# Optimization experiments

Measured on AMD Instinct MI355X. Metric: run time of the kernel, lower is better.

The kernel has to match this reference:

```python
import jax, jax.numpy as jnp
import numpy as np

N = 50000; E = 800000; G = 256; F = 34; D = 128; H = 4; C = 32; L = 4
EPS = 1e-5

def _bn(x, g, b):
    # BatchNorm1d with batch statistics (train-mode math), eval dropout (identity)
    m = jnp.mean(x, 0); v = jnp.var(x, 0)
    return g * (x - m) * jax.lax.rsqrt(v + EPS) + b

def _seg_softmax(s, seg, n):
    # numerically-stable softmax over edges grouped by destination node
    m = jax.ops.segment_max(s, seg, num_segments=n)
    m = jnp.where(jnp.isfinite(m), m, 0.0)
    e = jnp.exp(s - m[seg])
    d = jax.ops.segment_sum(e, seg, num_segments=n)
    return e / (d[seg] + 1e-16)

def setup_inputs():
    key = jax.random.key(0)
    ks = iter(jax.random.split(key, 64))
    def rn(shape, s=0.05):
        return jax.random.normal(next(ks), shape, dtype=jnp.float32) * s
    inp = {}
    inp['x'] = jax.random.normal(next(ks), (N, F), dtype=jnp.float32)
    inp['edge_index'] = jax.random.randint(next(ks), (2, E), 0, N, dtype=jnp.int32)
    inp['batch'] = jnp.sort(jax.random.randint(next(ks), (N,), 0, G, dtype=jnp.int32))
    inp['emb_W'] = rn((F, D)); inp['emb_b'] = rn((D,))
    inp['emb_g'] = jnp.ones((D,)); inp['emb_be'] = jnp.zeros((D,))
    inp['gWl'] = rn((L, D, D)); inp['gWr'] = rn((L, D, D))
    inp['gbl'] = rn((L, D)); inp['gbr'] = rn((L, D))
    inp['gatt'] = rn((L, H, C)); inp['gbias'] = rn((L, D))
    inp['gg'] = jnp.ones((L, D)); inp['gbe'] = jnp.zeros((L, D))
    inp['tWq'] = rn((D, D)); inp['tWk'] = rn((D, D)); inp['tWv'] = rn((D, D)); inp['tWs'] = rn((D, D))
    inp['tbq'] = rn((D,)); inp['tbk'] = rn((D,)); inp['tbv'] = rn((D,)); inp['tbs'] = rn((D,))
    inp['tg'] = jnp.ones((D,)); inp['tbe'] = jnp.zeros((D,))
    inp['oW1'] = rn((2 * D, D)); inp['ob1'] = rn((D,))
    inp['og'] = jnp.ones((D,)); inp['obe'] = jnp.zeros((D,))
    inp['oW2'] = rn((D, D // 2)); inp['ob2'] = rn((D // 2,))
    inp['oW3'] = rn((D // 2, 1)); inp['ob3'] = rn((1,))
    return inp

def reference(x, edge_index, batch, emb_W, emb_b, emb_g, emb_be, gWl, gWr, gbl, gbr, gatt, gbias, gg, gbe, tWq, tWk, tWv, tWs, tbq, tbk, tbv, tbs, tg, tbe, oW1, ob1, og, obe, oW2, ob2, oW3, ob3):
    x = jax.nn.relu(_bn(x @ emb_W + emb_b, emb_g, emb_be))
    sl = jnp.arange(N, dtype=edge_index.dtype)
    ei = jnp.concatenate([edge_index, jnp.stack([sl, sl])], axis=1)  # GATv2 default add_self_loops=True
    src, dst = ei[0], ei[1]
    for l in range(L):  # 4 structurally identical GATv2 layers
        xl = (x @ gWl[l] + gbl[l]).reshape(N, H, C)
        xr = (x @ gWr[l] + gbr[l]).reshape(N, H, C)
        e = jax.nn.leaky_relu(xl[src] + xr[dst], 0.2)  # [E+N, H, C]
        sc = jnp.einsum('ehc,hc->eh', e, gatt[l])
        a = _seg_softmax(sc, dst, N)
        out = jax.ops.segment_sum(xl[src] * a[..., None], dst, num_segments=N).reshape(N, D) + gbias[l]
        x = x + jax.nn.relu(_bn(out, gg[l], gbe[l]))
    # TransformerConv: no self-loops by default, dot-product attention + root skip
    s2, d2 = edge_index[0], edge_index[1]
    q = (x @ tWq + tbq).reshape(N, H, C)
    k = (x @ tWk + tbk).reshape(N, H, C)
    v = (x @ tWv + tbv).reshape(N, H, C)
    sc = jnp.einsum('ehc,ehc->eh', q[d2], k[s2]) / np.float32(np.sqrt(C))
    a = _seg_softmax(sc, d2, N)
    agg = jax.ops.segment_sum(v[s2] * a[..., None], d2, num_segments=N).reshape(N, D)
    x = x + _bn(agg + x @ tWs + tbs, tg, tbe)
    # global mean + max pooling over graphs
    cnt = jax.ops.segment_sum(jnp.ones((N,), x.dtype), batch, num_segments=G)
    xm = jax.ops.segment_sum(x, batch, num_segments=G) / jnp.maximum(cnt, 1.0)[:, None]
    xx = jax.ops.segment_max(x, batch, num_segments=G)
    xx = jnp.where(jnp.isfinite(xx), xx, 0.0)  # guard empty segments
    h = jnp.concatenate([xm, xx], axis=1)
    h = jax.nn.relu(_bn(h @ oW1 + ob1, og, obe))
    h = jax.nn.relu(h @ oW2 + ob2)
    return h @ oW3 + ob3
```

## Files before the change

kernel.cpp:

```cpp
#include <hip/hip_runtime.h>
#include <hip/hip_fp16.h>

namespace {
constexpr int NN = 50000;
constexpr int NE = 800000;
constexpr int NG = 256;
constexpr int NF = 34;
constexpr int NL = 4;
constexpr int NB = (NN + 255) / 256;
}
#define EPSB 1e-5f
#define LSLOPE 0.2f
#define INV_SQRT_C 0.17677669529663687f

typedef short bf16x8 __attribute__((ext_vector_type(8)));
typedef float f32x4 __attribute__((ext_vector_type(4)));
typedef _Float16 hv2 __attribute__((ext_vector_type(2)));

static __device__ __forceinline__ short f2bf(float f) {
    unsigned int u = __float_as_uint(f);
    u = (u + 0x7fff + ((u >> 16) & 1)) >> 16;
    return (short)u;
}
static __device__ __forceinline__ unsigned fenc(float x) {
    unsigned u = __float_as_uint(x);
    return (u & 0x80000000u) ? ~u : (u | 0x80000000u);
}
static __device__ __forceinline__ float fdec(unsigned u) {
    return __uint_as_float((u & 0x80000000u) ? (u ^ 0x80000000u) : ~u);
}
static __device__ __forceinline__ float fdot2(hv2 a, hv2 b, float c) {
    return __builtin_amdgcn_fdot2(a, b, c, false);
}

__global__ __launch_bounds__(256) void k_deg(const int* __restrict__ ei,
                                             int* __restrict__ deg,
                                             int* __restrict__ rank) {
    int tid = blockIdx.x * 256 + threadIdx.x;
    const int S = (NE + 3) / 4;
    if (tid >= S) return;
#pragma unroll
    for (int k = 0; k < 4; ++k) {
// ... 22 lines not shown
    sm[t] = v;
    __syncthreads();
    for (int off = 1; off < 256; off <<= 1) {
        int u = (t >= off) ? sm[t - off] : 0;
        __syncthreads();
        sm[t] += u;
        __syncthreads();
    }
    if (t < NB) boff[t] = sm[t] - v;
    if (t == 255) rp[NN] = sm[255];
}

__global__ __launch_bounds__(256) void k_scan3(const int* __restrict__ deg,
                                               const int* __restrict__ boff,
                                               int* __restrict__ rp) {
    __shared__ int sm[256];
    int i = blockIdx.x * 256 + threadIdx.x;
    int t = threadIdx.x;
    int v = (i < NN) ? deg[i] : 0;
    sm[t] = v;
    __syncthreads();
    for (int off = 1; off < 256; off <<= 1) {
        int u = (t >= off) ? sm[t - off] : 0;
        __syncthreads();
        sm[t] += u;
        __syncthreads();
    }
    if (i < NN) rp[i] = boff[blockIdx.x] + sm[t] - v;
}

__global__ __launch_bounds__(256) void k_fill(const int* __restrict__ ei,
                                              const int* __restrict__ rp,
                                              const int* __restrict__ rank,
                                              int2* __restrict__ edg) {
    int tid = blockIdx.x * 256 + threadIdx.x;
    const int S = (NE + 3) / 4;
    if (tid >= S) return;
#pragma unroll
    for (int k = 0; k < 4; ++k) {
        int e = tid + k * S;
        if (e < NE) {
            int s = ei[e];
            int d = ei[NE + e];
            int p = rp[d] + rank[e];
            edg[p] = make_int2(s, d);
        }
    }
}

__global__ __launch_bounds__(256) void k_prep(const float* __restrict__ gWl,
                                              const float* __restrict__ gWr,
                                              const float* __restrict__ tWq,
                                              const float* __restrict__ tWk,
                                              const float* __restrict__ tWv,
                                              const float* __restrict__ tWs,
                                              short* __restrict__ dst) {
    int m = blockIdx.x;
    const float* src;
    if (m < 4) src = gWl + m * 16384;
    else if (m < 8) src = gWr + (m - 4) * 16384;
    else if (m == 8) src = tWq;
    else if (m == 9) src = tWk;
    else if (m == 10) src = tWv;
    else src = tWs;
    short* d = dst + m * 16384;
    for (int i = threadIdx.x; i < 16384; i += 256) {
        int n = i >> 7, k = i & 127;
        d[i] = f2bf(src[k * 128 + n]);
    }
}

template <int OUTH0, int OUTH1, int RES, int XOUT>
__global__ __launch_bounds__(256) void k_gemm2bn(const float* __restrict__ src,
                                                 const float* __restrict__ res,
                                                 float* __restrict__ xout,
                                                 const float* __restrict__ st,
                                                 const float* __restrict__ g,
                                                 const float* __restrict__ b,
                                                 const short* __restrict__ Wt0,
                                                 const short* __restrict__ Wt1,
                                                 const float* __restrict__ bias0,
                                                 const float* __restrict__ bias1,
                                                 void* __restrict__ out0,
                                                 void* __restrict__ out1, int nRows) {
    __shared__ short As[128 * 136];
    __shared__ short Bs[128 * 136];
    __shared__ float scsh[256];
    const float invn = 1.f / NN;
    if (threadIdx.x < 128) {
        int c = threadIdx.x;
        float mean = st[c] * invn;
        float var = fmaxf(st[128 + c] * invn - mean * mean, 0.f);
        float s = g[c] * rsqrtf(var + EPSB);
        scsh[c] = s;
        scsh[128 + c] = b[c] - mean * s;
    }
    {
        const int4* Wt4 = (const int4*)Wt0;
        for (int idx = threadIdx.x; idx < 2048; idx += 256) {
            int row = idx >> 4, c8 = idx & 15;
            *(int4*)&Bs[row * 136 + c8 * 8] = Wt4[idx];
        }
    }
    __syncthreads();
    int r0 = blockIdx.x * 128;
    int rows = nRows - r0; if (rows > 128) rows = 128;
    for (int idx = threadIdx.x; idx < 2048; idx += 256) {
        int r = idx >> 4, c8 = idx & 15;
        short4 sa = {0, 0, 0, 0}, sb = {0, 0, 0, 0};
        if (r < rows) {
            size_t base = (size_t)(r0 + r) * 128 + c8 * 8;
            float4 v0 = *(const float4*)&src[base];
            float4 v1 = *(const float4*)&src[base + 4];
            int c = c8 * 8;
            v0.x = fmaxf(v0.x * scsh[c + 0] + scsh[128 + c + 0], 0.f);
            v0.y = fmaxf(v0.y * scsh[c + 1] + scsh[128 + c + 1], 0.f);
            v0.z = fmaxf(v0.z * scsh[c + 2] + scsh[128 + c + 2], 0.f);
            v0.w = fmaxf(v0.w * scsh[c + 3] + scsh[128 + c + 3], 0.f);
            v1.x = fmaxf(v1.x * scsh[c + 4] + scsh[128 + c + 4], 0.f);
            v1.y = fmaxf(v1.y * scsh[c + 5] + scsh[128 + c + 5], 0.f);
            v1.z = fmaxf(v1.z * scsh[c + 6] + scsh[128 + c + 6], 0.f);
            v1.w = fmaxf(v1.w * scsh[c + 7] + scsh[128 + c + 7], 0.f);
            if (RES) {
                float4 rr0 = *(const float4*)&res[base];
                float4 rr1 = *(const float4*)&res[base + 4];
// ... 79 lines not shown
#pragma unroll
            for (int reg = 0; reg < 4; ++reg) {
                int r = wave * 32 + rt * 16 + quad * 4 + reg;
                if (r < rows) {
                    float v = acc[rt][ct][reg] + bv;
                    if (OUTH1) ((__half*)out1)[(size_t)(r0 + r) * 128 + colI] = __float2half(v);
                    else       ((float*)out1)[(size_t)(r0 + r) * 128 + colI] = v;
                }
            }
    }
}

__global__ __launch_bounds__(256) void k_gemm4bn(const float* __restrict__ src,
                                                 const float* __restrict__ res,
                                                 float* __restrict__ xout,
                                                 const float* __restrict__ st,
                                                 const float* __restrict__ g,
                                                 const float* __restrict__ b,
                                                 const short* __restrict__ Wt,
                                                 const float* __restrict__ bq,
                                                 const float* __restrict__ bk,
                                                 const float* __restrict__ bv,
                                                 const float* __restrict__ bs,
                                                 __half* __restrict__ oq,
                                                 __half* __restrict__ ok,
                                                 __half* __restrict__ ov,
                                                 __half* __restrict__ os, int nRows) {
    __shared__ short As[128 * 136];
    __shared__ short Bs[128 * 136];
    __shared__ float scsh[256];
    const float invn = 1.f / NN;
    if (threadIdx.x < 128) {
        int c = threadIdx.x;
        float mean = st[c] * invn;
        float var = fmaxf(st[128 + c] * invn - mean * mean, 0.f);
        float s = g[c] * rsqrtf(var + EPSB);
        scsh[c] = s;
        scsh[128 + c] = b[c] - mean * s;
    }
    __syncthreads();
    int r0 = blockIdx.x * 128;
    int rows = nRows - r0; if (rows > 128) rows = 128;
    for (int idx = threadIdx.x; idx < 2048; idx += 256) {
        int r = idx >> 4, c8 = idx & 15;
        short4 sa = {0, 0, 0, 0}, sb = {0, 0, 0, 0};
        if (r < rows) {
            size_t base = (size_t)(r0 + r) * 128 + c8 * 8;
            float4 v0 = *(const float4*)&src[base];
            float4 v1 = *(const float4*)&src[base + 4];
            int c = c8 * 8;
            v0.x = fmaxf(v0.x * scsh[c + 0] + scsh[128 + c + 0], 0.f);
            v0.y = fmaxf(v0.y * scsh[c + 1] + scsh[128 + c + 1], 0.f);
            v0.z = fmaxf(v0.z * scsh[c + 2] + scsh[128 + c + 2], 0.f);
            v0.w = fmaxf(v0.w * scsh[c + 3] + scsh[128 + c + 3], 0.f);
            v1.x = fmaxf(v1.x * scsh[c + 4] + scsh[128 + c + 4], 0.f);
            v1.y = fmaxf(v1.y * scsh[c + 5] + scsh[128 + c + 5], 0.f);
            v1.z = fmaxf(v1.z * scsh[c + 6] + scsh[128 + c + 6], 0.f);
            v1.w = fmaxf(v1.w * scsh[c + 7] + scsh[128 + c + 7], 0.f);
            float4 rr0 = *(const float4*)&res[base];
            float4 rr1 = *(const float4*)&res[base + 4];
            v0.x += rr0.x; v0.y += rr0.y; v0.z += rr0.z; v0.w += rr0.w;
            v1.x += rr1.x; v1.y += rr1.y; v1.z += rr1.z; v1.w += rr1.w;
            *(float4*)&xout[base] = v0;
            *(float4*)&xout[base + 4] = v1;
            sa.x = f2bf(v0.x); sa.y = f2bf(v0.y); sa.z = f2bf(v0.z); sa.w = f2bf(v0.w);
            sb.x = f2bf(v1.x); sb.y = f2bf(v1.y); sb.z = f2bf(v1.z); sb.w = f2bf(v1.w);
        }
        *(short4*)&As[r * 136 + c8 * 8] = sa;
// ... 27 lines not shown
        for (int rt = 0; rt < 2; ++rt)
#pragma unroll
            for (int ct = 0; ct < 8; ++ct) acc[rt][ct] = (f32x4){0.f, 0.f, 0.f, 0.f};
#pragma unroll
        for (int ct = 0; ct < 8; ++ct)
#pragma unroll
            for (int kc = 0; kc < 4; ++kc) {
                bf16x8 bf = *(const bf16x8*)&Bs[(ct * 16 + n16) * 136 + kc * 32 + quad * 8];
                acc[0][ct] = __builtin_amdgcn_mfma_f32_16x16x32_bf16(af[0][kc], bf, acc[0][ct], 0, 0, 0);
                acc[1][ct] = __builtin_amdgcn_mfma_f32_16x16x32_bf16(af[1][kc], bf, acc[1][ct], 0, 0, 0);
            }
        __half* om = outs[m];
        const float* bm = biases[m];
#pragma unroll
        for (int ct = 0; ct < 8; ++ct) {
            int colI = ct * 16 + n16;
            float bv2 = bm[colI];
#pragma unroll
            for (int rt = 0; rt < 2; ++rt)
#pragma unroll
                for (int reg = 0; reg < 4; ++reg) {
                    int r = wave * 32 + rt * 16 + quad * 4 + reg;
                    if (r < rows)
                        om[(size_t)(r0 + r) * 128 + colI] = __float2half(acc[rt][ct][reg] + bv2);
                }
        }
        if (m < 3) __syncthreads();
    }
}

__global__ __launch_bounds__(256) void k_gemm_emb(const float* __restrict__ A,
                                                  const float* __restrict__ W,
                                                  const float* __restrict__ bias,
                                                  float* __restrict__ out, int nRows) {
    __shared__ float As[64 * NF];
    int r0 = blockIdx.x * 64;
    int rows = nRows - r0; if (rows > 64) rows = 64;
    int total = rows * NF;
    for (int idx = threadIdx.x; idx < 64 * NF; idx += 256)
        As[idx] = (idx < total) ? A[(size_t)r0 * NF + idx] : 0.f;
    __syncthreads();
    int tx = threadIdx.x & 31, ty = threadIdx.x >> 5;
    const float4* W4 = (const float4*)W;
    float acc[8][4];
#pragma unroll
    for (int j = 0; j < 8; ++j)
#pragma unroll
        for (int i = 0; i < 4; ++i) acc[j][i] = 0.f;
#pragma unroll 2
    for (int k = 0; k < NF; ++k) {
        float4 w = W4[k * 32 + tx];
#pragma unroll
        for (int j = 0; j < 8; ++j) {
            float a = As[(ty * 8 + j) * NF + k];
            acc[j][0] += a * w.x; acc[j][1] += a * w.y;
            acc[j][2] += a * w.z; acc[j][3] += a * w.w;
        }
    }
    float4 b = ((const float4*)bias)[tx];
#pragma unroll
    for (int j = 0; j < 8; ++j) {
        int r = ty * 8 + j;
        if (r < rows) {
            float4 o = make_float4(acc[j][0] + b.x, acc[j][1] + b.y,
                                   acc[j][2] + b.z, acc[j][3] + b.w);
            ((float4*)out)[(size_t)(r0 + r) * 32 + tx] = o;
        }
    }
}

__global__ __launch_bounds__(256) void k_stats(const float* __restrict__ src, int nRows,
                                               float* __restrict__ st) {
    int c = threadIdx.x & 127;
    int sub = threadIdx.x >> 7;
    int r0 = blockIdx.x * 128;
    int rend = r0 + 128; if (rend > nRows) rend = nRows;
    float s = 0.f, ss = 0.f;
    for (int r = r0 + sub; r < rend; r += 2) {
        float v = src[(size_t)r * 128 + c];
        s += v; ss += v * v;
    }
    atomicAdd(&st[c], s);
    atomicAdd(&st[128 + c], ss);
}

__global__ __launch_bounds__(256) void k_gat_aggr(const __half* __restrict__ xl,
                                                  const __half* __restrict__ xr,
                                                  const float* __restrict__ att,
                                                  const float* __restrict__ gbias_l,
                                                  const int* __restrict__ rp,
                                                  const int2* __restrict__ edg,
                                                  float* __restrict__ out) {
    int lane = threadIdx.x & 63;
    int node = blockIdx.x * 4 + (threadIdx.x >> 6);
    if (node >= NN) return;
    int q = lane >> 4;
    int l16 = lane & 15;
    int c8 = l16 * 8;
    float4 xrr = *(const float4*)&xr[(unsigned)node * 128u + c8];
    hv2 xrh[4] = {*(hv2*)&xrr.x, *(hv2*)&xrr.y, *(hv2*)&xrr.z, *(hv2*)&xrr.w};
    float4 atA = *(const float4*)&att[c8];
    float4 atB = *(const float4*)&att[c8 + 4];
    hv2 ath[4] = {{(_Float16)atA.x, (_Float16)atA.y}, {(_Float16)atA.z, (_Float16)atA.w},
                  {(_Float16)atB.x, (_Float16)atB.y}, {(_Float16)atB.z, (_Float16)atB.w}};
    const hv2 hz = {(_Float16)0.f, (_Float16)0.f};
    const hv2 hs = {(_Float16)LSLOPE, (_Float16)LSLOPE};
    int s0 = rp[node];
    int T = rp[node + 1] - s0 + 1;
    float a[8] = {0.f, 0.f, 0.f, 0.f, 0.f, 0.f, 0.f, 0.f};
    float l = 0.f;
    auto body = [&](int j) {
        bool self = (j == T - 1);
        int src = self ? node : edg[s0 + j].x;
        float4 raw = *(const float4*)&xl[(unsigned)src * 128u + c8];
        hv2 f[4] = {*(hv2*)&raw.x, *(hv2*)&raw.y, *(hv2*)&raw.z, *(hv2*)&raw.w};
        float p = 0.f;
#pragma unroll
        for (int k = 0; k < 4; ++k) {
            hv2 e = f[k] + xrh[k];
            hv2 lk = __builtin_elementwise_max(e, hz) + hs * __builtin_elementwise_min(e, hz);
            p = fdot2(lk, ath[k], p);
        }
        p += __shfl_xor(p, 1); p += __shfl_xor(p, 2);
        float w = __expf(p);
#pragma unroll
        for (int k = 0; k < 4; ++k) {
            a[2 * k] += w * (float)f[k].x;
            a[2 * k + 1] += w * (float)f[k].y;
        }
        l += w;
    };
    int j = q;
    for (; j + 4 < T; j += 8) { body(j); body(j + 4); }
    for (; j < T; j += 4) body(j);
#pragma unroll
    for (int k = 0; k < 8; ++k) { a[k] += __shfl_xor(a[k], 16); a[k] += __shfl_xor(a[k], 32); }
    l += __shfl_xor(l, 16); l += __shfl_xor(l, 32);
    if (q == 0) {
        float inv = 1.f / (l + 1e-16f);
        float4 gb0 = *(const float4*)&gbias_l[c8];
        float4 gb1 = *(const float4*)&gbias_l[c8 + 4];
        float4 o0 = make_float4(a[0] * inv + gb0.x, a[1] * inv + gb0.y,
                                a[2] * inv + gb0.z, a[3] * inv + gb0.w);
        float4 o1 = make_float4(a[4] * inv + gb1.x, a[5] * inv + gb1.y,
                                a[6] * inv + gb1.z, a[7] * inv + gb1.w);
        *(float4*)&out[(unsigned)node * 128u + c8] = o0;
        *(float4*)&out[(unsigned)node * 128u + c8 + 4] = o1;
    }
}

__global__ __launch_bounds__(256) void k_trans_aggr(const __half* __restrict__ qh,
                                                    const __half* __restrict__ kh,
                                                    const __half* __restrict__ vv,
                                                    const __half* __restrict__ sT,
                                                    const int* __restrict__ rp,
                                                    const int2* __restrict__ edg,
                                                    float* __restrict__ out) {
    int lane = threadIdx.x & 63;
    int node = blockIdx.x * 4 + (threadIdx.x >> 6);
    if (node >= NN) return;
    int q = lane >> 4;
    int l16 = lane & 15;
    int c8 = l16 * 8;
    float4 qr = *(const float4*)&qh[(unsigned)node * 128u + c8];
    const hv2 hinv = {(_Float16)INV_SQRT_C, (_Float16)INV_SQRT_C};
    hv2 qv[4] = {(*(hv2*)&qr.x) * hinv, (*(hv2*)&qr.y) * hinv,
                 (*(hv2*)&qr.z) * hinv, (*(hv2*)&qr.w) * hinv};
    int s0 = rp[node];
    int T = rp[node + 1] - s0;
    float a[8] = {0.f, 0.f, 0.f, 0.f, 0.f, 0.f, 0.f, 0.f};
    float l = 0.f;
    auto body = [&](int j) {
        int src = edg[s0 + j].x;
        float4 kraw = *(const float4*)&kh[(unsigned)src * 128u + c8];
        float4 vraw = *(const float4*)&vv[(unsigned)src * 128u + c8];
        hv2 kv[4] = {*(hv2*)&kraw.x, *(hv2*)&kraw.y, *(hv2*)&kraw.z, *(hv2*)&kraw.w};
        float p = 0.f;
#pragma unroll
        for (int k = 0; k < 4; ++k) p = fdot2(kv[k], qv[k], p);
        p += __shfl_xor(p, 1); p += __shfl_xor(p, 2);
        float w = __expf(p);
        hv2 vvv[4] = {*(hv2*)&vraw.x, *(hv2*)&vraw.y, *(hv2*)&vraw.z, *(hv2*)&vraw.w};
#pragma unroll
        for (int k = 0; k < 4; ++k) {
            a[2 * k] += w * (float)vvv[k].x;
            a[2 * k + 1] += w * (float)vvv[k].y;
        }
        l += w;
    };
    int j = q;
    for (; j + 4 < T; j += 8) { body(j); body(j + 4); }
    for (; j < T; j += 4) body(j);
#pragma unroll
    for (int k = 0; k < 8; ++k) { a[k] += __shfl_xor(a[k], 16); a[k] += __shfl_xor(a[k], 32); }
    l += __shfl_xor(l, 16); l += __shfl_xor(l, 32);
    if (q == 0) {
        float inv = 1.f / (l + 1e-16f);
        float4 straw = *(const float4*)&sT[(unsigned)node * 128u + c8];
        hv2 st[4] = {*(hv2*)&straw.x, *(hv2*)&straw.y, *(hv2*)&straw.z, *(hv2*)&straw.w};
        float4 o0 = make_float4(a[0] * inv + (float)st[0].x, a[1] * inv + (float)st[0].y,
                                a[2] * inv + (float)st[1].x, a[3] * inv + (float)st[1].y);
        float4 o1 = make_float4(a[4] * inv + (float)st[2].x, a[5] * inv + (float)st[2].y,
                                a[6] * inv + (float)st[3].x, a[7] * inv + (float)st[3].y);
        *(float4*)&out[(unsigned)node * 128u + c8] = o0;
        *(float4*)&out[(unsigned)node * 128u + c8 + 4] = o1;
    }
}

__global__ __launch_bounds__(256) void k_pool_part(const float* __restrict__ src,
                                                   const float* __restrict__ res,
                                                   const float* __restrict__ st,
                                                   const float* __restrict__ g,
                                                   const float* __restrict__ b,
                                                   const int* __restrict__ batch,
                                                   float* __restrict__ psum,
                                                   unsigned* __restrict__ pmax) {
    __shared__ int bs[64];
    int r0 = blockIdx.x * 64;
    if (threadIdx.x < 64) {
        int r = r0 + threadIdx.x;
        bs[threadIdx.x] = (r < NN) ? batch[r] : -1;
    }
    __syncthreads();
    int c = threadIdx.x & 127;
    int sub = threadIdx.x >> 7;
    const float invn = 1.f / NN;
    float mean = st[c] * invn;
    float var = fmaxf(st[128 + c] * invn - mean * mean, 0.f);
    float scv = g[c] * rsqrtf(var + EPSB);
    float shv = b[c] - mean * scv;
    int curg = -1;
    float s = 0.f, fmx = -INFINITY;
    for (int i = sub; i < 64; i += 2) {
        int r = r0 + i;
        if (r >= NN) break;
        int gr = bs[i];
        if (gr != curg) {
            if (curg >= 0) {
                atomicAdd(&psum[curg * 128 + c], s);
                atomicMax(&pmax[curg * 128 + c], fenc(fmx));
            }
            curg = gr; s = 0.f; fmx = -INFINITY;
        }
        float v = src[(size_t)r * 128 + c] * scv + shv + res[(size_t)r * 128 + c];
        s += v; fmx = fmaxf(fmx, v);
    }
    if (curg >= 0) {
        atomicAdd(&psum[curg * 128 + c], s);
        atomicMax(&pmax[curg * 128 + c], fenc(fmx));
    }
}

__global__ __launch_bounds__(128) void k_pool_final(const float* __restrict__ psum,
                                                    const unsigned* __restrict__ pmax,
                                                    const int* __restrict__ batch,
                                                    float* __restrict__ h) {
    __shared__ int se[2];
    int g = blockIdx.x;
    if (threadIdx.x == 0) {
        int lo = 0, hi = NN;
        while (lo < hi) { int mid = (lo + hi) >> 1; if (batch[mid] < g) lo = mid + 1; else hi = mid; }
        se[0] = lo;
        hi = NN;
        while (lo < hi) { int mid = (lo + hi) >> 1; if (batch[mid] < g + 1) lo = mid + 1; else hi = mid; }
        se[1] = lo;
    }
    __syncthreads();
    int cnt = se[1] - se[0];
    int c = threadIdx.x;
    float xm = psum[g * 128 + c] / fmaxf((float)cnt, 1.f);
    float xx = (cnt > 0) ? fdec(pmax[g * 128 + c]) : 0.f;
    h[g * 256 + c] = xm;
    h[g * 256 + 128 + c] = xx;
}

__global__ __launch_bounds__(128) void k_head1(const float* __restrict__ h,
                                               const float* __restrict__ W,
                                               const float* __restrict__ b,
                                               float* __restrict__ t1) {
    __shared__ float hr[256];
    int row = blockIdx.x;
    int t = threadIdx.x;
    hr[t] = h[row * 256 + t];
    hr[t + 128] = h[row * 256 + 128 + t];
    __syncthreads();
    float acc = b[t];
#pragma unroll 4
    for (int k = 0; k < 256; ++k) acc += hr[k] * W[k * 128 + t];
    t1[row * 128 + t] = acc;
}

__global__ __launch_bounds__(64) void k_head2(const float* __restrict__ t1,
                                              const float* __restrict__ st,
                                              const float* __restrict__ og,
                                              const float* __restrict__ obe,
                                              const float* __restrict__ W2,
                                              const float* __restrict__ b2,
                                              const float* __restrict__ W3,
                                              const float* __restrict__ b3,
                                              float* __restrict__ out) {
    __shared__ float v[128];
    int row = blockIdx.x, t = threadIdx.x;
    const float invn = 1.f / NG;
#pragma unroll
    for (int half = 0; half < 2; ++half) {
        int ch = t + half * 64;
        float mean = st[ch] * invn;
        float var = fmaxf(st[128 + ch] * invn - mean * mean, 0.f);
        float scv = og[ch] * rsqrtf(var + EPSB);
        float shv = obe[ch] - mean * scv;
        float a = t1[row * 128 + ch] * scv + shv;
        v[ch] = fmaxf(a, 0.f);
    }
    __syncthreads();
    float acc = b2[t];
#pragma unroll 4
    for (int k = 0; k < 128; ++k) acc += v[k] * W2[k * 64 + t];
    float p = fmaxf(acc, 0.f) * W3[t];
    p += __shfl_xor(p, 1); p += __shfl_xor(p, 2); p += __shfl_xor(p, 4);
    p += __shfl_xor(p, 8); p += __shfl_xor(p, 16); p += __shfl_xor(p, 32);
    if (t == 0) out[row] = p + b3[0];
}
// ... 28 lines not shown
    const float* tbe    = (const float*)d_in[24];
    const float* oW1    = (const float*)d_in[25];
    const float* ob1    = (const float*)d_in[26];
    const float* og     = (const float*)d_in[27];
    const float* obe    = (const float*)d_in[28];
    const float* oW2    = (const float*)d_in[29];
    const float* ob2    = (const float*)d_in[30];
    const float* oW3    = (const float*)d_in[31];
    const float* ob3    = (const float*)d_in[32];
    float* out = (float*)d_out;

    const size_t NDsz = (size_t)NN * 128;
    float* x     = (float*)d_ws;
    float* bA    = x + NDsz;
    float* bC    = bA + NDsz;
    float* stats = bC + NDsz;
    float* hpool = stats + 7 * 256;
    float* t1    = hpool + 65536;
    float* scb   = t1 + 32768;
    __half* xlh  = (__half*)(scb + (size_t)(NE + NN) * 4);
    __half* xrh  = xlh + NDsz;
    __half* vh   = xrh + NDsz;
    __half* sh   = vh + NDsz;
    short* Wt    = (short*)(sh + NDsz);
    int* deg     = (int*)(Wt + 12 * 16384);
    int* rp      = deg + NN;
    int* cursor  = rp + NN + 1;
    int2* edg    = (int2*)(cursor + NN);
    int* bsum    = (int*)(edg + NE + 64);
    int* boff    = bsum + 256;
    float* psum  = (float*)(boff + 256);
    unsigned* pmax = (unsigned*)(psum + NG * 128);
    int* rank    = (int*)scb;

    hipMemsetAsync(deg, 0, NN * sizeof(int), stream);
    hipMemsetAsync(stats, 0, 7 * 256 * sizeof(float), stream);
    hipMemsetAsync(psum, 0, NG * 128 * 2 * sizeof(float), stream);

    k_prep<<<12, 256, 0, stream>>>(gWl, gWr, tWq, tWk, tWv, tWs, Wt);

    const int S4 = (NE + 3) / 4;
    const int gQuarter = (S4 + 255) / 256;
    k_deg<<<gQuarter, 256, 0, stream>>>(ei, deg, rank);
    k_scan1<<<NB, 256, 0, stream>>>(deg, bsum);
    k_scan2<<<1, 256, 0, stream>>>(bsum, boff, rp);
    k_scan3<<<NB, 256, 0, stream>>>(deg, boff, rp);
    k_fill<<<gQuarter, 256, 0, stream>>>(ei, rp, rank, edg);

    const int gEmb  = (NN + 63) / 64;
    const int gGemm = (NN + 127) / 128;
    const int gStat = (NN + 127) / 128;
    const int gNode = (NN + 3) / 4;
    const int gPool = (NN + 63) / 64;

    k_gemm_emb<<<gEmb, 256, 0, stream>>>(x_in, emb_W, emb_b, bA, NN);
    k_stats<<<gStat, 256, 0, stream>>>(bA, NN, stats);

    k_gemm2bn<1, 1, 0, 1><<<gGemm, 256, 0, stream>>>(bA, nullptr, x, stats, emb_g, emb_be,
                                                     Wt + (size_t)0 * 16384, Wt + (size_t)4 * 16384,
                                                     gbl + 0 * 128, gbr + 0 * 128, xlh, xrh, NN);
    k_gat_aggr<<<gNode, 256, 0, stream>>>(xlh, xrh, gatt + 0 * 128, gbias + 0 * 128, rp, edg, bC);
    k_stats<<<gStat, 256, 0, stream>>>(bC, NN, stats + 1 * 256);
    k_gemm2bn<1, 1, 1, 1><<<gGemm, 256, 0, stream>>>(bC, x, bA, stats + 1 * 256, gg + 0 * 128, gbe + 0 * 128,
                                                     Wt + (size_t)1 * 16384, Wt + (size_t)5 * 16384,
                                                     gbl + 1 * 128, gbr + 1 * 128, xlh, xrh, NN);
    k_gat_aggr<<<gNode, 256, 0, stream>>>(xlh, xrh, gatt + 1 * 128, gbias + 1 * 128, rp, edg, bC);
    k_stats<<<gStat, 256, 0, stream>>>(bC, NN, stats + 2 * 256);
    k_gemm2bn<1, 1, 1, 1><<<gGemm, 256, 0, stream>>>(bC, bA, x, stats + 2 * 256, gg + 1 * 128, gbe + 1 * 128,
                                                     Wt + (size_t)2 * 16384, Wt + (size_t)6 * 16384,
                                                     gbl + 2 * 128, gbr + 2 * 128, xlh, xrh, NN);
    k_gat_aggr<<<gNode, 256, 0, stream>>>(xlh, xrh, gatt + 2 * 128, gbias + 2 * 128, rp, edg, bC);
    k_stats<<<gStat, 256, 0, stream>>>(bC, NN, stats + 3 * 256);
    k_gemm2bn<1, 1, 1, 1><<<gGemm, 256, 0, stream>>>(bC, x, bA, stats + 3 * 256, gg + 2 * 128, gbe + 2 * 128,
                                                     Wt + (size_t)3 * 16384, Wt + (size_t)7 * 16384,
                                                     gbl + 3 * 128, gbr + 3 * 128, xlh, xrh, NN);
    k_gat_aggr<<<gNode, 256, 0, stream>>>(xlh, xrh, gatt + 3 * 128, gbias + 3 * 128, rp, edg, bC);
    k_stats<<<gStat, 256, 0, stream>>>(bC, NN, stats + 4 * 256);

    k_gemm4bn<<<gGemm, 256, 0, stream>>>(bC, bA, x, stats + 4 * 256, gg + 3 * 128, gbe + 3 * 128,
                                         Wt + (size_t)8 * 16384, tbq, tbk, tbv, tbs,
                                         xrh, xlh, vh, sh, NN);
    k_trans_aggr<<<gNode, 256, 0, stream>>>(xrh, xlh, vh, sh, rp, edg, bC);
    k_stats<<<gStat, 256, 0, stream>>>(bC, NN, stats + 5 * 256);

    k_pool_part<<<gPool, 256, 0, stream>>>(bC, x, stats + 5 * 256, tg, tbe, batch, psum, pmax);
    k_pool_final<<<NG, 128, 0, stream>>>(psum, pmax, batch, hpool);
    k_head1<<<NG, 128, 0, stream>>>(hpool, oW1, ob1, t1);
    k_stats<<<(NG + 127) / 128, 256, 0, stream>>>(t1, NG, stats + 6 * 256);
    k_head2<<<NG, 64, 0, stream>>>(t1, stats + 6 * 256, og, obe, oW2, ob2, oW3, ob3, out);
}
```

Before: 921.9 us.

## Fuse BatchNorm statistics into producer kernels and compact edge list

Removes the separate k_stats passes by accumulating per-channel sum and sum-of-squares inside the embedding GEMM, GAT aggregation, transformer aggregation and head1 kernels. Partial sums are spread over 32 strided slots to reduce atomic contention, and consumers reduce those slots. The CSR edge array stores only source indices, which the aggregation kernels load 64 at a time and broadcast by shuffle. Pool-final and head1 are merged. This saves re-reading the 50000x128 activations several times and some launches, at the cost of extra shared-memory atomics and a block-wide sync in the aggregation kernels.

```diff
diff --git a/kernel.cpp b/kernel.cpp
--- a/kernel.cpp
+++ b/kernel.cpp
@@ -8,6 +8,7 @@
 constexpr int NF = 34;
 constexpr int NL = 4;
 constexpr int NB = (NN + 255) / 256;
+constexpr int STS = 32;
 }
 #define EPSB 1e-5f
 #define LSLOPE 0.2f
@@ -96,7 +97,7 @@
 __global__ __launch_bounds__(256) void k_fill(const int* __restrict__ ei,
                                               const int* __restrict__ rp,
                                               const int* __restrict__ rank,
-                                              int2* __restrict__ edg) {
+                                              int* __restrict__ esrc) {
     int tid = blockIdx.x * 256 + threadIdx.x;
     const int S = (NE + 3) / 4;
     if (tid >= S) return;
@@ -107,7 +108,7 @@
             int s = ei[e];
             int d = ei[NE + e];
             int p = rp[d] + rank[e];
-            edg[p] = make_int2(s, d);
+            esrc[p] = s;
         }
     }
 }
@@ -153,8 +154,14 @@
     const float invn = 1.f / NN;
     if (threadIdx.x < 128) {
         int c = threadIdx.x;
-        float mean = st[c] * invn;
-        float var = fmaxf(st[128 + c] * invn - mean * mean, 0.f);
+        float s0v = 0.f, s1v = 0.f;
+#pragma unroll 8
+        for (int k2 = 0; k2 < STS; ++k2) {
+            s0v += st[k2 * 256 + c];
+            s1v += st[k2 * 256 + 128 + c];
+        }
+        float mean = s0v * invn;
+        float var = fmaxf(s1v * invn - mean * mean, 0.f);
         float s = g[c] * rsqrtf(var + EPSB);
         scsh[c] = s;
         scsh[128 + c] = b[c] - mean * s;
@@ -300,8 +307,14 @@
     const float invn = 1.f / NN;
     if (threadIdx.x < 128) {
         int c = threadIdx.x;
-        float mean = st[c] * invn;
-        float var = fmaxf(st[128 + c] * invn - mean * mean, 0.f);
+        float s0v = 0.f, s1v = 0.f;
+#pragma unroll 8
+        for (int k2 = 0; k2 < STS; ++k2) {
+            s0v += st[k2 * 256 + c];
+            s1v += st[k2 * 256 + 128 + c];
+        }
+        float mean = s0v * invn;
+        float var = fmaxf(s1v * invn - mean * mean, 0.f);
         float s = g[c] * rsqrtf(var + EPSB);
         scsh[c] = s;
         scsh[128 + c] = b[c] - mean * s;
@@ -395,13 +408,16 @@
 __global__ __launch_bounds__(256) void k_gemm_emb(const float* __restrict__ A,
                                                   const float* __restrict__ W,
                                                   const float* __restrict__ bias,
-                                                  float* __restrict__ out, int nRows) {
+                                                  float* __restrict__ out, int nRows,
+                                                  float* __restrict__ stms) {
     __shared__ float As[64 * NF];
+    __shared__ float sred[256];
     int r0 = blockIdx.x * 64;
     int rows = nRows - r0; if (rows > 64) rows = 64;
     int total = rows * NF;
     for (int idx = threadIdx.x; idx < 64 * NF; idx += 256)
         As[idx] = (idx < total) ? A[(size_t)r0 * NF + idx] : 0.f;
+    sred[threadIdx.x] = 0.f;
     __syncthreads();
     int tx = threadIdx.x & 31, ty = threadIdx.x >> 5;
     const float4* W4 = (const float4*)W;
@@ -421,6 +437,7 @@
         }
     }
     float4 b = ((const float4*)bias)[tx];
+    float s[4] = {0.f, 0.f, 0.f, 0.f}, ss[4] = {0.f, 0.f, 0.f, 0.f};
 #pragma unroll
     for (int j = 0; j < 8; ++j) {
         int r = ty * 8 + j;
@@ -428,23 +445,19 @@
             float4 o = make_float4(acc[j][0] + b.x, acc[j][1] + b.y,
                                    acc[j][2] + b.z, acc[j][3] + b.w);
             ((float4*)out)[(size_t)(r0 + r) * 32 + tx] = o;
-        }
-    }
-}
-
-__global__ __launch_bounds__(256) void k_stats(const float* __restrict__ src, int nRows,
-                                               float* __restrict__ st) {
-    int c = threadIdx.x & 127;
-    int sub = threadIdx.x >> 7;
-    int r0 = blockIdx.x * 128;
-    int rend = r0 + 128; if (rend > nRows) rend = nRows;
-    float s = 0.f, ss = 0.f;
-    for (int r = r0 + sub; r < rend; r += 2) {
-        float v = src[(size_t)r * 128 + c];
-        s += v; ss += v * v;
-    }
-    atomicAdd(&st[c], s);
-    atomicAdd(&st[128 + c], ss);
+            s[0] += o.x; ss[0] += o.x * o.x;
+            s[1] += o.y; ss[1] += o.y * o.y;
+            s[2] += o.z; ss[2] += o.z * o.z;
+            s[3] += o.w; ss[3] += o.w * o.w;
+        }
+    }
+#pragma unroll
+    for (int i = 0; i < 4; ++i) {
+        atomicAdd(&sred[tx * 4 + i], s[i]);
+        atomicAdd(&sred[128 + tx * 4 + i], ss[i]);
+    }
+    __syncthreads();
+    atomicAdd(&stms[(blockIdx.x & (STS - 1)) * 256 + threadIdx.x], sred[threadIdx.x]);
 }
 
 __global__ __launch_bounds__(256) void k_gat_aggr(const __half* __restrict__ xl,
@@ -452,64 +465,85 @@
                                                   const float* __restrict__ att,
                                                   const float* __restrict__ gbias_l,
                                                   const int* __restrict__ rp,
-                                                  const int2* __restrict__ edg,
-                                                  float* __restrict__ out) {
+                                                  const int* __restrict__ esrc,
+                                                  float* __restrict__ out,
+                                                  float* __restrict__ stms) {
+    __shared__ float smst[256];
+    smst[threadIdx.x] = 0.f;
+    __syncthreads();
     int lane = threadIdx.x & 63;
     int node = blockIdx.x * 4 + (threadIdx.x >> 6);
-    if (node >= NN) return;
     int q = lane >> 4;
     int l16 = lane & 15;
     int c8 = l16 * 8;
-    float4 xrr = *(const float4*)&xr[(unsigned)node * 128u + c8];
-    hv2 xrh[4] = {*(hv2*)&xrr.x, *(hv2*)&xrr.y, *(hv2*)&xrr.z, *(hv2*)&xrr.w};
-    float4 atA = *(const float4*)&att[c8];
-    float4 atB = *(const float4*)&att[c8 + 4];
-    hv2 ath[4] = {{(_Float16)atA.x, (_Float16)atA.y}, {(_Float16)atA.z, (_Float16)atA.w},
-                  {(_Float16)atB.x, (_Float16)atB.y}, {(_Float16)atB.z, (_Float16)atB.w}};
-    const hv2 hz = {(_Float16)0.f, (_Float16)0.f};
-    const hv2 hs = {(_Float16)LSLOPE, (_Float16)LSLOPE};
-    int s0 = rp[node];
-    int T = rp[node + 1] - s0 + 1;
-    float a[8] = {0.f, 0.f, 0.f, 0.f, 0.f, 0.f, 0.f, 0.f};
-    float l = 0.f;
-    auto body = [&](int j) {
-        bool self = (j == T - 1);
-        int src = self ? node : edg[s0 + j].x;
-        float4 raw = *(const float4*)&xl[(unsigned)src * 128u + c8];
-        hv2 f[4] = {*(hv2*)&raw.x, *(hv2*)&raw.y, *(hv2*)&raw.z, *(hv2*)&raw.w};
-        float p = 0.f;
-#pragma unroll
-        for (int k = 0; k < 4; ++k) {
-            hv2 e = f[k] + xrh[k];
-            hv2 lk = __builtin_elementwise_max(e, hz) + hs * __builtin_elementwise_min(e, hz);
-            p = fdot2(lk, ath[k], p);
-        }
-        p += __shfl_xor(p, 1); p += __shfl_xor(p, 2);
-        float w = __expf(p);
-#pragma unroll
-        for (int k = 0; k < 4; ++k) {
-            a[2 * k] += w * (float)f[k].x;
-            a[2 * k + 1] += w * (float)f[k].y;
-        }
-        l += w;
-    };
-    int j = q;
-    for (; j + 4 < T; j += 8) { body(j); body(j + 4); }
-    for (; j < T; j += 4) body(j);
-#pragma unroll
-    for (int k = 0; k < 8; ++k) { a[k] += __shfl_xor(a[k], 16); a[k] += __shfl_xor(a[k], 32); }
-    l += __shfl_xor(l, 16); l += __shfl_xor(l, 32);
-    if (q == 0) {
-        float inv = 1.f / (l + 1e-16f);
-        float4 gb0 = *(const float4*)&gbias_l[c8];
-        float4 gb1 = *(const float4*)&gbias_l[c8 + 4];
-        float4 o0 = make_float4(a[0] * inv + gb0.x, a[1] * inv + gb0.y,
-                                a[2] * inv + gb0.z, a[3] * inv + gb0.w);
-        float4 o1 = make_float4(a[4] * inv + gb1.x, a[5] * inv + gb1.y,
-                                a[6] * inv + gb1.z, a[7] * inv + gb1.w);
-        *(float4*)&out[(unsigned)node * 128u + c8] = o0;
-        *(float4*)&out[(unsigned)node * 128u + c8 + 4] = o1;
-    }
+    if (node < NN) {
+        float4 xrr = *(const float4*)&xr[(unsigned)node * 128u + c8];
+        hv2 xrv[4] = {*(hv2*)&xrr.x, *(hv2*)&xrr.y, *(hv2*)&xrr.z, *(hv2*)&xrr.w};
+        float4 atA = *(const float4*)&att[c8];
+        float4 atB = *(const float4*)&att[c8 + 4];
+        hv2 ath[4] = {{(_Float16)atA.x, (_Float16)atA.y}, {(_Float16)atA.z, (_Float16)atA.w},
+                      {(_Float16)atB.x, (_Float16)atB.y}, {(_Float16)atB.z, (_Float16)atB.w}};
+        const hv2 hz = {(_Float16)0.f, (_Float16)0.f};
+        const hv2 hs = {(_Float16)LSLOPE, (_Float16)LSLOPE};
+        int s0 = rp[node];
+        int T = rp[node + 1] - s0 + 1;
+        float a[8] = {0.f, 0.f, 0.f, 0.f, 0.f, 0.f, 0.f, 0.f};
+        float l = 0.f;
+        for (int base = 0; base < T; base += 64) {
+            int eidx = esrc[s0 + base + lane];
+            int rem = T - base; if (rem > 64) rem = 64;
+            int jend = base + rem;
+            int iters = (rem + 3) >> 2;
+            auto step = [&](int j) {
+                int srcn = __shfl(eidx, j - base, 64);
+                if (j < jend) {
+                    if (j == T - 1) srcn = node;
+                    float4 raw = *(const float4*)&xl[(unsigned)srcn * 128u + c8];
+                    hv2 f[4] = {*(hv2*)&raw.x, *(hv2*)&raw.y, *(hv2*)&raw.z, *(hv2*)&raw.w};
+                    float p = 0.f;
+#pragma unroll
+                    for (int k = 0; k < 4; ++k) {
+                        hv2 e = f[k] + xrv[k];
+                        hv2 lk = __builtin_elementwise_max(e, hz) + hs * __builtin_elementwise_min(e, hz);
+                        p = fdot2(lk, ath[k], p);
+                    }
+                    p += __shfl_xor(p, 1); p += __shfl_xor(p, 2);
+                    float w = __expf(p);
+#pragma unroll
+                    for (int k = 0; k < 4; ++k) {
+                        a[2 * k] += w * (float)f[k].x;
+                        a[2 * k + 1] += w * (float)f[k].y;
+                    }
+                    l += w;
+                }
+            };
+            int j = base + q, it = 0;
+            for (; it + 1 < iters; it += 2) { step(j); step(j + 4); j += 8; }
+            if (it < iters) step(j);
+        }
+#pragma unroll
+        for (int k = 0; k < 8; ++k) { a[k] += __shfl_xor(a[k], 16); a[k] += __shfl_xor(a[k], 32); }
+        l += __shfl_xor(l, 16); l += __shfl_xor(l, 32);
+        if (q == 0) {
+            float inv = 1.f / (l + 1e-16f);
+            float4 gb0 = *(const float4*)&gbias_l[c8];
+            float4 gb1 = *(const float4*)&gbias_l[c8 + 4];
+            float o[8];
+            o[0] = a[0] * inv + gb0.x; o[1] = a[1] * inv + gb0.y;
+            o[2] = a[2] * inv + gb0.z; o[3] = a[3] * inv + gb0.w;
+            o[4] = a[4] * inv + gb1.x; o[5] = a[5] * inv + gb1.y;
+            o[6] = a[6] * inv + gb1.z; o[7] = a[7] * inv + gb1.w;
+            *(float4*)&out[(unsigned)node * 128u + c8] = make_float4(o[0], o[1], o[2], o[3]);
+            *(float4*)&out[(unsigned)node * 128u + c8 + 4] = make_float4(o[4], o[5], o[6], o[7]);
+#pragma unroll
+            for (int k = 0; k < 8; ++k) {
+                atomicAdd(&smst[c8 + k], o[k]);
+                atomicAdd(&smst[128 + c8 + k], o[k] * o[k]);
+            }
+        }
+    }
+    __syncthreads();
+    atomicAdd(&stms[(blockIdx.x & (STS - 1)) * 256 + threadIdx.x], smst[threadIdx.x]);
 }
 
 __global__ __launch_bounds__(256) void k_trans_aggr(const __half* __restrict__ qh,
@@ -517,57 +551,78 @@
                                                     const __half* __restrict__ vv,
                                                     const __half* __restrict__ sT,
                                                     const int* __restrict__ rp,
-                                                    const int2* __restrict__ edg,
-                                                    float* __restrict__ out) {
+                                                    const int* __restrict__ esrc,
+                                                    float* __restrict__ out,
+                                                    float* __restrict__ stms) {
+    __shared__ float smst[256];
+    smst[threadIdx.x] = 0.f;
+    __syncthreads();
     int lane = threadIdx.x & 63;
     int node = blockIdx.x * 4 + (threadIdx.x >> 6);
-    if (node >= NN) return;
     int q = lane >> 4;
     int l16 = lane & 15;
     int c8 = l16 * 8;
-    float4 qr = *(const float4*)&qh[(unsigned)node * 128u + c8];
-    const hv2 hinv = {(_Float16)INV_SQRT_C, (_Float16)INV_SQRT_C};
-    hv2 qv[4] = {(*(hv2*)&qr.x) * hinv, (*(hv2*)&qr.y) * hinv,
-                 (*(hv2*)&qr.z) * hinv, (*(hv2*)&qr.w) * hinv};
-    int s0 = rp[node];
-    int T = rp[node + 1] - s0;
-    float a[8] = {0.f, 0.f, 0.f, 0.f, 0.f, 0.f, 0.f, 0.f};
-    float l = 0.f;
-    auto body = [&](int j) {
-        int src = edg[s0 + j].x;
-        float4 kraw = *(const float4*)&kh[(unsigned)src * 128u + c8];
-        float4 vraw = *(const float4*)&vv[(unsigned)src * 128u + c8];
-        hv2 kv[4] = {*(hv2*)&kraw.x, *(hv2*)&kraw.y, *(hv2*)&kraw.z, *(hv2*)&kraw.w};
-        float p = 0.f;
-#pragma unroll
-        for (int k = 0; k < 4; ++k) p = fdot2(kv[k], qv[k], p);
-        p += __shfl_xor(p, 1); p += __shfl_xor(p, 2);
-        float w = __expf(p);
-        hv2 vvv[4] = {*(hv2*)&vraw.x, *(hv2*)&vraw.y, *(hv2*)&vraw.z, *(hv2*)&vraw.w};
-#pragma unroll
-        for (int k = 0; k < 4; ++k) {
-            a[2 * k] += w * (float)vvv[k].x;
-            a[2 * k + 1] += w * (float)vvv[k].y;
-        }
-        l += w;
-    };
-    int j = q;
-    for (; j + 4 < T; j += 8) { body(j); body(j + 4); }
-    for (; j < T; j += 4) body(j);
-#pragma unroll
-    for (int k = 0; k < 8; ++k) { a[k] += __shfl_xor(a[k], 16); a[k] += __shfl_xor(a[k], 32); }
-    l += __shfl_xor(l, 16); l += __shfl_xor(l, 32);
-    if (q == 0) {
-        float inv = 1.f / (l + 1e-16f);
-        float4 straw = *(const float4*)&sT[(unsigned)node * 128u + c8];
-        hv2 st[4] = {*(hv2*)&straw.x, *(hv2*)&straw.y, *(hv2*)&straw.z, *(hv2*)&straw.w};
-        float4 o0 = make_float4(a[0] * inv + (float)st[0].x, a[1] * inv + (float)st[0].y,
-                                a[2] * inv + (float)st[1].x, a[3] * inv + (float)st[1].y);
-        float4 o1 = make_float4(a[4] * inv + (float)st[2].x, a[5] * inv + (float)st[2].y,
-                                a[6] * inv + (float)st[3].x, a[7] * inv + (float)st[3].y);
-        *(float4*)&out[(unsigned)node * 128u + c8] = o0;
-        *(float4*)&out[(unsigned)node * 128u + c8 + 4] = o1;
-    }
+    if (node < NN) {
+        float4 qr = *(const float4*)&qh[(unsigned)node * 128u + c8];
+        const hv2 hinv = {(_Float16)INV_SQRT_C, (_Float16)INV_SQRT_C};
+        hv2 qv[4] = {(*(hv2*)&qr.x) * hinv, (*(hv2*)&qr.y) * hinv,
+                     (*(hv2*)&qr.z) * hinv, (*(hv2*)&qr.w) * hinv};
+        int s0 = rp[node];
+        int T = rp[node + 1] - s0;
+        float a[8] = {0.f, 0.f, 0.f, 0.f, 0.f, 0.f, 0.f, 0.f};
+        float l = 0.f;
+        for (int base = 0; base < T; base += 64) {
+            int eidx = esrc[s0 + base + lane];
+            int rem = T - base; if (rem > 64) rem = 64;
+            int jend = base + rem;
+            int iters = (rem + 3) >> 2;
+            auto step = [&](int j) {
+                int srcn = __shfl(eidx, j - base, 64);
+                if (j < jend) {
+                    float4 kraw = *(const float4*)&kh[(unsigned)srcn * 128u + c8];
+                    float4 vraw = *(const float4*)&vv[(unsigned)srcn * 128u + c8];
+                    hv2 kv[4] = {*(hv2*)&kraw.x, *(hv2*)&kraw.y, *(hv2*)&kraw.z, *(hv2*)&kraw.w};
+                    float p = 0.f;
+#pragma unroll
+                    for (int k = 0; k < 4; ++k) p = fdot2(kv[k], qv[k], p);
+                    p += __shfl_xor(p, 1); p += __shfl_xor(p, 2);
+                    float w = __expf(p);
+                    hv2 vvv[4] = {*(hv2*)&vraw.x, *(hv2*)&vraw.y, *(hv2*)&vraw.z, *(hv2*)&vraw.w};
+#pragma unroll
+                    for (int k = 0; k < 4; ++k) {
+                        a[2 * k] += w * (float)vvv[k].x;
+                        a[2 * k + 1] += w * (float)vvv[k].y;
+                    }
+                    l += w;
+                }
+            };
+            int j = base + q, it = 0;
+            for (; it + 1 < iters; it += 2) { step(j); step(j + 4); j += 8; }
+            if (it < iters) step(j);
+        }
+#pragma unroll
+        for (int k = 0; k < 8; ++k) { a[k] += __shfl_xor(a[k], 16); a[k] += __shfl_xor(a[k], 32); }
+        l += __shfl_xor(l, 16); l += __shfl_xor(l, 32);
+        if (q == 0) {
+            float inv = 1.f / (l + 1e-16f);
+            float4 straw = *(const float4*)&sT[(unsigned)node * 128u + c8];
+            hv2 st[4] = {*(hv2*)&straw.x, *(hv2*)&straw.y, *(hv2*)&straw.z, *(hv2*)&straw.w};
+            float o[8];
+            o[0] = a[0] * inv + (float)st[0].x; o[1] = a[1] * inv + (float)st[0].y;
+            o[2] = a[2] * inv + (float)st[1].x; o[3] = a[3] * inv + (float)st[1].y;
+            o[4] = a[4] * inv + (float)st[2].x; o[5] = a[5] * inv + (float)st[2].y;
+            o[6] = a[6] * inv + (float)st[3].x; o[7] = a[7] * inv + (float)st[3].y;
+            *(float4*)&out[(unsigned)node * 128u + c8] = make_float4(o[0], o[1], o[2], o[3]);
+            *(float4*)&out[(unsigned)node * 128u + c8 + 4] = make_float4(o[4], o[5], o[6], o[7]);
+#pragma unroll
+            for (int k = 0; k < 8; ++k) {
+                atomicAdd(&smst[c8 + k], o[k]);
+                atomicAdd(&smst[128 + c8 + k], o[k] * o[k]);
+            }
+        }
+    }
+    __syncthreads();
+    atomicAdd(&stms[(blockIdx.x & (STS - 1)) * 256 + threadIdx.x], smst[threadIdx.x]);
 }
 
 __global__ __launch_bounds__(256) void k_pool_part(const float* __restrict__ src,
@@ -579,19 +634,32 @@
                                                    float* __restrict__ psum,
                                                    unsigned* __restrict__ pmax) {
     __shared__ int bs[64];
+    __shared__ float sc_sh[128], sh_sh[128];
     int r0 = blockIdx.x * 64;
     if (threadIdx.x < 64) {
         int r = r0 + threadIdx.x;
         bs[threadIdx.x] = (r < NN) ? batch[r] : -1;
     }
+    const float invn = 1.f / NN;
+    if (threadIdx.x < 128) {
+        int c2 = threadIdx.x;
+        float s0v = 0.f, s1v = 0.f;
+#pragma unroll 8
+        for (int k2 = 0; k2 < STS; ++k2) {
+            s0v += st[k2 * 256 + c2];
+            s1v += st[k2 * 256 + 128 + c2];
+        }
+        float mean = s0v * invn;
+        float var = fmaxf(s1v * invn - mean * mean, 0.f);
+        float scv = g[c2] * rsqrtf(var + EPSB);
+        sc_sh[c2] = scv;
+        sh_sh[c2] = b[c2] - mean * scv;
+    }
     __syncthreads();
     int c = threadIdx.x & 127;
     int sub = threadIdx.x >> 7;
-    const float invn = 1.f / NN;
-    float mean = st[c] * invn;
-    float var = fmaxf(st[128 + c] * invn - mean * mean, 0.f);
-    float scv = g[c] * rsqrtf(var + EPSB);
-    float shv = b[c] - mean * scv;
+    float scv = sc_sh[c];
+    float shv = sh_sh[c];
     int curg = -1;
     float s = 0.f, fmx = -INFINITY;
     for (int i = sub; i < 64; i += 2) {
@@ -614,13 +682,18 @@
     }
 }
 
-__global__ __launch_bounds__(128) void k_pool_final(const float* __restrict__ psum,
+__global__ __launch_bounds__(128) void k_pool_head1(const float* __restrict__ psum,
                                                     const unsigned* __restrict__ pmax,
                                                     const int* __restrict__ batch,
-                                                    float* __restrict__ h) {
+                                                    const float* __restrict__ W,
+                                                    const float* __restrict__ b,
+                                                    float* __restrict__ t1,
+                                                    float* __restrict__ st6) {
+    __shared__ float hr[256];
     __shared__ int se[2];
     int g = blockIdx.x;
-    if (threadIdx.x == 0) {
+    int t = threadIdx.x;
+    if (t == 0) {
         int lo = 0, hi = NN;
         while (lo < hi) { int mid = (lo + hi) >> 1; if (batch[mid] < g) lo = mid + 1; else hi = mid; }
         se[0] = lo;
@@ -630,27 +703,17 @@
     }
     __syncthreads();
     int cnt = se[1] - se[0];
-    int c = threadIdx.x;
-    float xm = psum[g * 128 + c] / fmaxf((float)cnt, 1.f);
-    float xx = (cnt > 0) ? fdec(pmax[g * 128 + c]) : 0.f;
-    h[g * 256 + c] = xm;
-    h[g * 256 + 128 + c] = xx;
-}
-
-__global__ __launch_bounds__(128) void k_head1(const float* __restrict__ h,
-                                               const float* __restrict__ W,
-                                               const float* __restrict__ b,
-                                               float* __restrict__ t1) {
-    __shared__ float hr[256];
-    int row = blockIdx.x;
-    int t = threadIdx.x;
-    hr[t] = h[row * 256 + t];
-    hr[t + 128] = h[row * 256 + 128 + t];
+    float xm = psum[g * 128 + t] / fmaxf((float)cnt, 1.f);
+    float xx = (cnt > 0) ? fdec(pmax[g * 128 + t]) : 0.f;
+    hr[t] = xm;
+    hr[128 + t] = xx;
     __syncthreads();
     float acc = b[t];
 #pragma unroll 4
     for (int k = 0; k < 256; ++k) acc += hr[k] * W[k * 128 + t];
-    t1[row * 128 + t] = acc;
+    t1[g * 128 + t] = acc;
+    atomicAdd(&st6[t], acc);
+    atomicAdd(&st6[128 + t], acc * acc);
 }
 
 __global__ __launch_bounds__(64) void k_head2(const float* __restrict__ t1,
@@ -745,9 +808,12 @@
     float* psum  = (float*)(boff + 256);
     unsigned* pmax = (unsigned*)(psum + NG * 128);
     int* rank    = (int*)scb;
+    int* esrc    = (int*)edg;
+    float* stms  = scb + NE;
 
     hipMemsetAsync(deg, 0, NN * sizeof(int), stream);
-    hipMemsetAsync(stats, 0, 7 * 256 * sizeof(float), stream);
+    hipMemsetAsync(stats + 6 * 256, 0, 256 * sizeof(float), stream);
+    hipMemsetAsync(stms, 0, 6 * STS * 256 * sizeof(float), stream);
     hipMemsetAsync(psum, 0, NG * 128 * 2 * sizeof(float), stream);
 
     k_prep<<<12, 256, 0, stream>>>(gWl, gWr, tWq, tWk, tWv, tWs, Wt);
@@ -758,47 +824,39 @@
     k_scan1<<<NB, 256, 0, stream>>>(deg, bsum);
     k_scan2<<<1, 256, 0, stream>>>(bsum, boff, rp);
     k_scan3<<<NB, 256, 0, stream>>>(deg, boff, rp);
-    k_fill<<<gQuarter, 256, 0, stream>>>(ei, rp, rank, edg);
+    k_fill<<<gQuarter, 256, 0, stream>>>(ei, rp, rank, esrc);
 
     const int gEmb  = (NN + 63) / 64;
     const int gGemm = (NN + 127) / 128;
-    const int gStat = (NN + 127) / 128;
     const int gNode = (NN + 3) / 4;
     const int gPool = (NN + 63) / 64;
-
-    k_gemm_emb<<<gEmb, 256, 0, stream>>>(x_in, emb_W, emb_b, bA, NN);
-    k_stats<<<gStat, 256, 0, stream>>>(bA, NN, stats);
-
-    k_gemm2bn<1, 1, 0, 1><<<gGemm, 256, 0, stream>>>(bA, nullptr, x, stats, emb_g, emb_be,
+    const int REG = STS * 256;
+
+    k_gemm_emb<<<gEmb, 256, 0, stream>>>(x_in, emb_W, emb_b, bA, NN, stms + 0 * REG);
+
+    k_gemm2bn<1, 1, 0, 1><<<gGemm, 256, 0, stream>>>(bA, nullptr, x, stms + 0 * REG, emb_g, emb_be,
                                                      Wt + (size_t)0 * 16384, Wt + (size_t)4 * 16384,
                                                      gbl + 0 * 128, gbr + 0 * 128, xlh, xrh, NN);
-    k_gat_aggr<<<gNode, 256, 0, stream>>>(xlh, xrh, gatt + 0 * 128, gbias + 0 * 128, rp, edg, bC);
-    k_stats<<<gStat, 256, 0, stream>>>(bC, NN, stats + 1 * 256);
-    k_gemm2bn<1, 1, 1, 1><<<gGemm, 256, 0, stream>>>(bC, x, bA, stats + 1 * 256, gg + 0 * 128, gbe + 0 * 128,
+    k_gat_aggr<<<gNode, 256, 0, stream>>>(xlh, xrh, gatt + 0 * 128, gbias + 0 * 128, rp, esrc, bC, stms + 1 * REG);
+    k_gemm2bn<1, 1, 1, 1><<<gGemm, 256, 0, stream>>>(bC, x, bA, stms + 1 * REG, gg + 0 * 128, gbe + 0 * 128,
                                                      Wt + (size_t)1 * 16384, Wt + (size_t)5 * 16384,
                                                      gbl + 1 * 128, gbr + 1 * 128, xlh, xrh, NN);
-    k_gat_aggr<<<gNode, 256, 0, stream>>>(xlh, xrh, gatt + 1 * 128, gbias + 1 * 128, rp, edg, bC);
-    k_stats<<<gStat, 256, 0, stream>>>(bC, NN, stats + 2 * 256);
-    k_gemm2bn<1, 1, 1, 1><<<gGemm, 256, 0, stream>>>(bC, bA, x, stats + 2 * 256, gg + 1 * 128, gbe + 1 * 128,
+    k_gat_aggr<<<gNode, 256, 0, stream>>>(xlh, xrh, gatt + 1 * 128, gbias + 1 * 128, rp, esrc, bC, stms + 2 * REG);
+    k_gemm2bn<1, 1, 1, 1><<<gGemm, 256, 0, stream>>>(bC, bA, x, stms + 2 * REG, gg + 1 * 128, gbe + 1 * 128,
                                                      Wt + (size_t)2 * 16384, Wt + (size_t)6 * 16384,
                                                      gbl + 2 * 128, gbr + 2 * 128, xlh, xrh, NN);
-    k_gat_aggr<<<gNode, 256, 0, stream>>>(xlh, xrh, gatt + 2 * 128, gbias + 2 * 128, rp, edg, bC);
-    k_stats<<<gStat, 256, 0, stream>>>(bC, NN, stats + 3 * 256);
-    k_gemm2bn<1, 1, 1, 1><<<gGemm, 256, 0, stream>>>(bC, x, bA, stats + 3 * 256, gg + 2 * 128, gbe + 2 * 128,
+    k_gat_aggr<<<gNode, 256, 0, stream>>>(xlh, xrh, gatt + 2 * 128, gbias + 2 * 128, rp, esrc, bC, stms + 3 * REG);
+    k_gemm2bn<1, 1, 1, 1><<<gGemm, 256, 0, stream>>>(bC, x, bA, stms + 3 * REG, gg + 2 * 128, gbe + 2 * 128,
                                                      Wt + (size_t)3 * 16384, Wt + (size_t)7 * 16384,
                                                      gbl + 3 * 128, gbr + 3 * 128, xlh, xrh, NN);
-    k_gat_aggr<<<gNode, 256, 0, stream>>>(xlh, xrh, gatt + 3 * 128, gbias + 3 * 128, rp, edg, bC);
-    k_stats<<<gStat, 256, 0, stream>>>(bC, NN, stats + 4 * 256);
-
-    k_gemm4bn<<<gGemm, 256, 0, stream>>>(bC, bA, x, stats + 4 * 256, gg + 3 * 128, gbe + 3 * 128,
+    k_gat_aggr<<<gNode, 256, 0, stream>>>(xlh, xrh, gatt + 3 * 128, gbias + 3 * 128, rp, esrc, bC, stms + 4 * REG);
+
+    k_gemm4bn<<<gGemm, 256, 0, stream>>>(bC, bA, x, stms + 4 * REG, gg + 3 * 128, gbe + 3 * 128,
                                          Wt + (size_t)8 * 16384, tbq, tbk, tbv, tbs,
                                          xrh, xlh, vh, sh, NN);
-    k_trans_aggr<<<gNode, 256, 0, stream>>>(xrh, xlh, vh, sh, rp, edg, bC);
-    k_stats<<<gStat, 256, 0, stream>>>(bC, NN, stats + 5 * 256);
-
-    k_pool_part<<<gPool, 256, 0, stream>>>(bC, x, stats + 5 * 256, tg, tbe, batch, psum, pmax);
-    k_pool_final<<<NG, 128, 0, stream>>>(psum, pmax, batch, hpool);
-    k_head1<<<NG, 128, 0, stream>>>(hpool, oW1, ob1, t1);
-    k_stats<<<(NG + 127) / 128, 256, 0, stream>>>(t1, NG, stats + 6 * 256);
+    k_trans_aggr<<<gNode, 256, 0, stream>>>(xrh, xlh, vh, sh, rp, esrc, bC, stms + 5 * REG);
+
+    k_pool_part<<<gPool, 256, 0, stream>>>(bC, x, stms + 5 * REG, tg, tbe, batch, psum, pmax);
+    k_pool_head1<<<NG, 128, 0, stream>>>(psum, pmax, batch, oW1, ob1, t1, stats + 6 * 256);
     k_head2<<<NG, 64, 0, stream>>>(t1, stats + 6 * 256, og, obe, oW2, ob2, oW3, ob3, out);
 }
```

New measurement: 928.0 us. Within noise of the previous version (+0.7%).
